# Optimization experiments

Hardware: AMD Instinct MI355X
Metric: run time of the kernel (lower is better)

## Reference

```python
import jax, jax.numpy as jnp
import numpy as np

B, H, W, C = 4, 64, 64, 256
D = C // 8  # out_channels // queries_ratio = 32


def setup_inputs() -> dict:
    key = jax.random.key(0)
    ks = jax.random.split(key, 8)
    s_in = 1.0 / np.sqrt(C)  # he_normal-ish scale for 1x1 convs
    s_d = 1.0 / np.sqrt(D)
    return {
        "x": jax.random.normal(ks[0], (B, H, W, C), dtype=jnp.float32),
        "Wk": jax.random.normal(ks[1], (C, D), dtype=jnp.float32) * s_in,
        "bk": jnp.zeros((D,), dtype=jnp.float32),
        "Wq": jax.random.normal(ks[2], (C, D), dtype=jnp.float32) * s_in,
        "bq": jnp.zeros((D,), dtype=jnp.float32),
        "Wv": jax.random.normal(ks[3], (C, D), dtype=jnp.float32) * s_in,
        "bv": jnp.zeros((D,), dtype=jnp.float32),
        "Wo": jax.random.normal(ks[4], (D, C), dtype=jnp.float32) * s_d,
        "bo": jnp.zeros((C,), dtype=jnp.float32),
        "gamma": jax.random.normal(ks[5], (1,), dtype=jnp.float32) * 0.1,
    }


def reference(x, Wk, bk, Wq, bq, Wv, bv, Wo, bo, gamma):
    b, h, w, c = x.shape
    n = h * w
    xf = x.reshape(b, n, c)  # flatten spatial -> [B, N, C]
    # 1x1 convs == per-position channel matmuls
    k = xf @ Wk + bk  # [B, N, D]
    q = xf @ Wq + bq  # [B, N, D]
    v = xf @ Wv + bv  # [B, N, D]
    energy = jnp.einsum('bnd,bmd->bnm', q, k)  # [B, N, N] (no scaling, as in source)
    attn = jax.nn.softmax(energy, axis=-1)
    feat = jnp.einsum('bnm,bmd->bnd', attn, v)  # [B, N, D]
    out = feat @ Wo + bo  # 1x1 output conv -> [B, N, C]
    out = gamma[0] * out + xf  # gamma scale + identity shortcut (C_in == C_out)
    return out.reshape(b, h, w, c)
```

## Files before the change

### kernel.cpp

```cpp
#include <hip/hip_runtime.h>
#include <hip/hip_bf16.h>
#include <hip/hip_fp16.h>


#define BB 4
#define NN 4096
#define CC 256
#define DD 32
#define LOG2E 1.44269504088896340736f
#define THR2 11.0f

typedef _Float16 half_t;
typedef _Float16 half2_t __attribute__((ext_vector_type(2)));
typedef _Float16 half4_t __attribute__((ext_vector_type(4)));
typedef _Float16 half8_t __attribute__((ext_vector_type(8)));
typedef float f32x4 __attribute__((ext_vector_type(4)));

#define MFMA_QK(a, b, c) __builtin_amdgcn_mfma_f32_16x16x32_f16(a, b, c, 0, 0, 0)
#define MFMA_PV(a, b, c) __builtin_amdgcn_mfma_f32_16x16x16f16(a, b, c, 0, 0, 0)

static __device__ inline float fexp2(float x) {
#if __has_builtin(__builtin_amdgcn_exp2f)
    return __builtin_amdgcn_exp2f(x);
#else
    return exp2f(x);
#endif
}

__global__ __launch_bounds__(256) void proj_kernel(
    const float* __restrict__ x,
    const float* __restrict__ Wk, const float* __restrict__ bk,
    const float* __restrict__ Wq, const float* __restrict__ bq,
    const float* __restrict__ Wv, const float* __restrict__ bv,
    half_t* __restrict__ k_ws, half_t* __restrict__ q_ws, half_t* __restrict__ vT2)
{
    __shared__ half_t xs16[32][264];
    __shared__ half_t Wt[96][264];

    const int t = threadIdx.x;
    const int row0 = blockIdx.x * 32;

    const float4* x4 = reinterpret_cast<const float4*>(x) + (size_t)row0 * 64;
    for (int idx = t; idx < 32 * 64; idx += 256) {
        int r = idx >> 6, c4 = idx & 63;
        float4 v = x4[r * 64 + c4];
        half4_t h;
        h[0] = (half_t)v.x; h[1] = (half_t)v.y; h[2] = (half_t)v.z; h[3] = (half_t)v.w;
        *reinterpret_cast<half4_t*>(&xs16[r][c4 * 4]) = h;
    }

    for (int idx = t; idx < 3072; idx += 256) {
        int cp = idx & 127;
        int rest = idx >> 7;
        int d4 = (rest & 7) * 4;
        int mat = rest >> 3;
        const float* Wm = (mat == 0) ? Wk : ((mat == 1) ? Wq : Wv);
        const float sc = (mat == 1) ? LOG2E : 1.0f;
        float4 w0 = *reinterpret_cast<const float4*>(Wm + (2 * cp) * DD + d4);
        float4 w1 = *reinterpret_cast<const float4*>(Wm + (2 * cp + 1) * DD + d4);
        int rbase = mat * 32 + d4;
        half2_t h;
        h[0] = (half_t)(w0.x * sc); h[1] = (half_t)(w1.x * sc);
        *reinterpret_cast<half2_t*>(&Wt[rbase + 0][2 * cp]) = h;
        h[0] = (half_t)(w0.y * sc); h[1] = (half_t)(w1.y * sc);
        *reinterpret_cast<half2_t*>(&Wt[rbase + 1][2 * cp]) = h;
        h[0] = (half_t)(w0.z * sc); h[1] = (half_t)(w1.z * sc);
        *reinterpret_cast<half2_t*>(&Wt[rbase + 2][2 * cp]) = h;
        h[0] = (half_t)(w0.w * sc); h[1] = (half_t)(w1.w * sc);
        *reinterpret_cast<half2_t*>(&Wt[rbase + 3][2 * cp]) = h;
    }
    __syncthreads();

    const int w = t >> 6, lane = t & 63;
    const int c = lane & 15, g = lane >> 4;
    const int rt = w >> 1;
    const int ct0 = (w & 1) * 3;

    f32x4 acc[3];
#pragma unroll
    for (int j = 0; j < 3; ++j) acc[j] = (f32x4){0.f, 0.f, 0.f, 0.f};

#pragma unroll
    for (int kk = 0; kk < 8; ++kk) {
        const int k0 = kk * 32 + g * 8;
        half8_t bfrag = *reinterpret_cast<const half8_t*>(&xs16[rt * 16 + c][k0]);
#pragma unroll
        for (int j = 0; j < 3; ++j) {
            half8_t afrag = *reinterpret_cast<const half8_t*>(&Wt[(ct0 + j) * 16 + c][k0]);
            acc[j] = MFMA_QK(afrag, bfrag, acc[j]);
        }
    }

    const int grow = row0 + rt * 16 + c;
#pragma unroll
    for (int j = 0; j < 3; ++j) {
        const int ct = ct0 + j;
        const int mat = ct >> 1;
        const float* bm = (mat == 0) ? bk : ((mat == 1) ? bq : bv);
        float4 bb = *reinterpret_cast<const float4*>(bm + (ct & 1) * 16 + g * 4);
        if (mat < 2) {
            const float bsc = (mat == 1) ? LOG2E : 1.0f;
            half_t* dst = (mat == 0) ? k_ws : q_ws;
            half4_t h;
            h[0] = (half_t)(acc[j][0] + bb.x * bsc);
            h[1] = (half_t)(acc[j][1] + bb.y * bsc);
            h[2] = (half_t)(acc[j][2] + bb.z * bsc);
            h[3] = (half_t)(acc[j][3] + bb.w * bsc);
            *reinterpret_cast<half4_t*>(dst + (size_t)grow * DD + (ct & 1) * 16 + g * 4) = h;
        } else {
            const size_t tbase = ((size_t)(row0 >> 4) + rt) * 512;
            const int d0 = (ct & 1) * 16 + g * 4;
            vT2[tbase + (size_t)(d0 + 0) * 16 + c] = (half_t)(acc[j][0] + bb.x);
            vT2[tbase + (size_t)(d0 + 1) * 16 + c] = (half_t)(acc[j][1] + bb.y);
            vT2[tbase + (size_t)(d0 + 2) * 16 + c] = (half_t)(acc[j][2] + bb.z);
            vT2[tbase + (size_t)(d0 + 3) * 16 + c] = (half_t)(acc[j][3] + bb.w);
        }
    }
}

__global__ __launch_bounds__(512) void attn_kernel(
    const half_t* __restrict__ k_ws, const half_t* __restrict__ q_ws,
    const half_t* __restrict__ vT2,
    const float* __restrict__ x, const float* __restrict__ Wo,
    const float* __restrict__ bo, const float* __restrict__ gamma,
    float* __restrict__ out)
{
    __shared__ float m_l[8][4][16];
    __shared__ float s_l[8][4][16];
    __shared__ float acc_l[8][64][4][8];
    __shared__ float feat_lds[64][32];

    const int tid = threadIdx.x;
    const int w = tid >> 6, lane = tid & 63;
    const int q = lane & 15, g = lane >> 4;
    const int b = blockIdx.x >> 6, qb = blockIdx.x & 63;
    const int q0 = qb * 64;

    half8_t qf[4];
#pragma unroll
    for (int t = 0; t < 4; ++t)
        qf[t] = *reinterpret_cast<const half8_t*>(
            q_ws + (size_t)(b * NN + q0 + t * 16 + q) * DD + g * 8);

    float m[4], ssum[4];
    f32x4 accd0[4], accd1[4];
#pragma unroll
    for (int t = 0; t < 4; ++t) {
        m[t] = -3.0e38f; ssum[t] = 0.f;
        accd0[t] = (f32x4){0.f, 0.f, 0.f, 0.f};
        accd1[t] = (f32x4){0.f, 0.f, 0.f, 0.f};
    }

    const half_t* kbase = k_ws + ((size_t)b * NN + q) * DD + g * 8;
    const half_t* vb = vT2 + (size_t)b * 256 * 512 + q * 16 + g * 4;

    const int ktbase = w * 32;

    half8_t kc0 = *reinterpret_cast<const half8_t*>(kbase + (size_t)(ktbase + 0) * 16 * DD);
    half8_t kc1 = *reinterpret_cast<const half8_t*>(kbase + (size_t)(ktbase + 1) * 16 * DD);
    half4_t va0 = *reinterpret_cast<const half4_t*>(vb + (size_t)(ktbase + 0) * 512);
    half4_t va1 = *reinterpret_cast<const half4_t*>(vb + (size_t)(ktbase + 0) * 512 + 256);
    half4_t vc0 = *reinterpret_cast<const half4_t*>(vb + (size_t)(ktbase + 1) * 512);
    half4_t vc1 = *reinterpret_cast<const half4_t*>(vb + (size_t)(ktbase + 1) * 512 + 256);

    for (int it = 0; it < 16; ++it) {
        const int kt = ktbase + it * 2;
        const int ktn = (it < 15) ? (kt + 2) : kt;

        half8_t kn0 = *reinterpret_cast<const half8_t*>(kbase + (size_t)(ktn + 0) * 16 * DD);
        half8_t kn1 = *reinterpret_cast<const half8_t*>(kbase + (size_t)(ktn + 1) * 16 * DD);
        half4_t wa0 = *reinterpret_cast<const half4_t*>(vb + (size_t)(ktn + 0) * 512);
        half4_t wa1 = *reinterpret_cast<const half4_t*>(vb + (size_t)(ktn + 0) * 512 + 256);
        half4_t wc0 = *reinterpret_cast<const half4_t*>(vb + (size_t)(ktn + 1) * 512);
        half4_t wc1 = *reinterpret_cast<const half4_t*>(vb + (size_t)(ktn + 1) * 512 + 256);

        f32x4 z = {0.f, 0.f, 0.f, 0.f};
        f32x4 s0[4], s1[4];
#pragma unroll
        for (int t = 0; t < 4; ++t) {
            s0[t] = MFMA_QK(kc0, qf[t], z);
            s1[t] = MFMA_QK(kc1, qf[t], z);
        }

        float tmax[4];
        bool need = false;
#pragma unroll
        for (int t = 0; t < 4; ++t) {
            float t0 = fmaxf(fmaxf(s0[t][0], s0[t][1]), fmaxf(s0[t][2], s0[t][3]));
            float t1 = fmaxf(fmaxf(s1[t][0], s1[t][1]), fmaxf(s1[t][2], s1[t][3]));
            tmax[t] = fmaxf(t0, t1);
            need = need || (tmax[t] > m[t] + THR2);
        }

        if (__any(need)) {
#pragma unroll
            for (int t = 0; t < 4; ++t) {
                float rmax = tmax[t];
                rmax = fmaxf(rmax, __shfl_xor(rmax, 16));
                rmax = fmaxf(rmax, __shfl_xor(rmax, 32));
                float mn = fmaxf(m[t], rmax);
                float sc = fexp2(m[t] - mn);
                ssum[t] *= sc;
                accd0[t] *= sc;
                accd1[t] *= sc;
                m[t] = mn;
            }
        }

#pragma unroll
        for (int t = 0; t < 4; ++t) {
            float p00 = fexp2(s0[t][0] - m[t]), p01 = fexp2(s0[t][1] - m[t]);
            float p02 = fexp2(s0[t][2] - m[t]), p03 = fexp2(s0[t][3] - m[t]);
            float p10 = fexp2(s1[t][0] - m[t]), p11 = fexp2(s1[t][1] - m[t]);
            float p12 = fexp2(s1[t][2] - m[t]), p13 = fexp2(s1[t][3] - m[t]);
            ssum[t] += ((p00 + p01) + (p02 + p03)) + ((p10 + p11) + (p12 + p13));

            half4_t pf0, pf1;
            pf0[0] = (half_t)p00; pf0[1] = (half_t)p01; pf0[2] = (half_t)p02; pf0[3] = (half_t)p03;
            pf1[0] = (half_t)p10; pf1[1] = (half_t)p11; pf1[2] = (half_t)p12; pf1[3] = (half_t)p13;

            accd0[t] = MFMA_PV(va0, pf0, accd0[t]);
            accd1[t] = MFMA_PV(va1, pf0, accd1[t]);
            accd0[t] = MFMA_PV(vc0, pf1, accd0[t]);
            accd1[t] = MFMA_PV(vc1, pf1, accd1[t]);
        }

        kc0 = kn0; kc1 = kn1;
        va0 = wa0; va1 = wa1; vc0 = wc0; vc1 = wc1;
    }

#pragma unroll
    for (int t = 0; t < 4; ++t) {
        ssum[t] += __shfl_xor(ssum[t], 16);
        ssum[t] += __shfl_xor(ssum[t], 32);
    }

    if (lane < 16) {
#pragma unroll
        for (int t = 0; t < 4; ++t) { m_l[w][t][lane] = m[t]; s_l[w][t][lane] = ssum[t]; }
    }
#pragma unroll
    for (int t = 0; t < 4; ++t)
#pragma unroll
        for (int i = 0; i < 4; ++i) {
            acc_l[w][lane][t][i] = accd0[t][i];
            acc_l[w][lane][t][4 + i] = accd1[t][i];
        }
    __syncthreads();

    if (w < 4) {
        const int t = w;
        float M = m_l[0][t][q];
#pragma unroll
        for (int ww = 1; ww < 8; ++ww) M = fmaxf(M, m_l[ww][t][q]);
        float SS = 0.f;
        float f[8] = {0.f, 0.f, 0.f, 0.f, 0.f, 0.f, 0.f, 0.f};
#pragma unroll
        for (int ww = 0; ww < 8; ++ww) {
            float sc = fexp2(m_l[ww][t][q] - M);
            SS += s_l[ww][t][q] * sc;
#pragma unroll
            for (int i = 0; i < 8; ++i) f[i] += acc_l[ww][lane][t][i] * sc;
        }
        float inv = 1.0f / SS;
#pragma unroll
        for (int i = 0; i < 4; ++i) {
            feat_lds[t * 16 + q][g * 4 + i] = f[i] * inv;
            feat_lds[t * 16 + q][16 + g * 4 + i] = f[4 + i] * inv;
        }
    }
    __syncthreads();

    const int c = tid & 255, rh = tid >> 8;
    float wv[32];
#pragma unroll
    for (int d = 0; d < DD; ++d) wv[d] = Wo[d * CC + c];
    const float gam = gamma[0];
    const float bias = bo[c];

#pragma unroll
    for (int chunk = 0; chunk < 4; ++chunk) {
        const int r0 = rh * 32 + chunk * 8;
        float oacc[8] = {0.f, 0.f, 0.f, 0.f, 0.f, 0.f, 0.f, 0.f};
#pragma unroll
        for (int d = 0; d < DD; ++d) {
            float wvd = wv[d];
#pragma unroll
            for (int r = 0; r < 8; ++r) oacc[r] += feat_lds[r0 + r][d] * wvd;
        }
        const size_t base = ((size_t)b * NN + (size_t)q0 + r0) * CC + c;
        const float* xr = x + base;
        float* outr = out + base;
#pragma unroll
        for (int r = 0; r < 8; ++r)
            outr[(size_t)r * CC] = gam * (oacc[r] + bias) + xr[(size_t)r * CC];
    }
}

extern "C" void kernel_launch(void* const* d_in, const int* in_sizes, int n_in,
                              void* d_out, int out_size, void* d_ws, size_t ws_size,
                              hipStream_t stream) {
    const float* x  = (const float*)d_in[0];
    const float* Wk = (const float*)d_in[1];
    const float* bk = (const float*)d_in[2];
    const float* Wq = (const float*)d_in[3];
    const float* bq = (const float*)d_in[4];
    const float* Wv = (const float*)d_in[5];
    const float* bv = (const float*)d_in[6];
    const float* Wo = (const float*)d_in[7];
    const float* bo = (const float*)d_in[8];
    const float* gamma = (const float*)d_in[9];
    float* out = (float*)d_out;

    half_t* k_ws  = (half_t*)d_ws;
    half_t* q_ws  = k_ws + (size_t)BB * NN * DD;
    half_t* vT2   = q_ws + (size_t)BB * NN * DD;

    proj_kernel<<<512, 256, 0, stream>>>(x, Wk, bk, Wq, bq, Wv, bv, k_ws, q_ws, vT2);
    attn_kernel<<<256, 512, 0, stream>>>(k_ws, q_ws, vT2, x, Wo, bo, gamma, out);
}
```

Before: 46.50 us.

## Use MFMA for output projection and double proj kernel rows per block

The attention epilogue now stages Wo transposed in fp16 in shared memory and computes the output 1x1 conv with 16x16x32 MFMA instructions instead of scalar FMAs. It also writes float4-vectorized output. The per-wave accumulator buffer is padded to reduce LDS bank conflicts. The projection kernel handles 64 rows per block with 512 threads, which halves the number of times the weights are staged. The costs are fp16 rounding of feat and Wo, extra LDS use, and the hidden proj compute loop must match the new thread count.

After: 40.38 us. 1.15x faster.

```diff
diff --git a/kernel.cpp b/kernel.cpp
--- a/kernel.cpp
+++ b/kernel.cpp
@@ -27,21 +27,21 @@
 #endif
 }
 
-__global__ __launch_bounds__(256) void proj_kernel(
+__global__ __launch_bounds__(512) void proj_kernel(
     const float* __restrict__ x,
     const float* __restrict__ Wk, const float* __restrict__ bk,
     const float* __restrict__ Wq, const float* __restrict__ bq,
     const float* __restrict__ Wv, const float* __restrict__ bv,
     half_t* __restrict__ k_ws, half_t* __restrict__ q_ws, half_t* __restrict__ vT2)
 {
-    __shared__ half_t xs16[32][264];
+    __shared__ half_t xs16[64][264];
     __shared__ half_t Wt[96][264];
 
     const int t = threadIdx.x;
-    const int row0 = blockIdx.x * 32;
+    const int row0 = blockIdx.x * 64;
 
     const float4* x4 = reinterpret_cast<const float4*>(x) + (size_t)row0 * 64;
-    for (int idx = t; idx < 32 * 64; idx += 256) {
+    for (int idx = t; idx < 64 * 64; idx += 512) {
         int r = idx >> 6, c4 = idx & 63;
         float4 v = x4[r * 64 + c4];
         half4_t h;
@@ -49,7 +49,7 @@
         *reinterpret_cast<half4_t*>(&xs16[r][c4 * 4]) = h;
     }
 
-    for (int idx = t; idx < 3072; idx += 256) {
+    for (int idx = t; idx < 3072; idx += 512) {
         int cp = idx & 127;
         int rest = idx >> 7;
         int d4 = (rest & 7) * 4;
@@ -125,16 +125,24 @@
     const float* __restrict__ bo, const float* __restrict__ gamma,
     float* __restrict__ out)
 {
+    __shared__ float acc_l[8][64][33];
     __shared__ float m_l[8][4][16];
     __shared__ float s_l[8][4][16];
-    __shared__ float acc_l[8][64][4][8];
-    __shared__ float feat_lds[64][32];
+    __shared__ half_t feat_h[64 * 40];
+    __shared__ half_t woT[256 * 40];
 
     const int tid = threadIdx.x;
     const int w = tid >> 6, lane = tid & 63;
     const int q = lane & 15, g = lane >> 4;
     const int b = blockIdx.x >> 6, qb = blockIdx.x & 63;
     const int q0 = qb * 64;
+
+#pragma unroll
+    for (int it = 0; it < 16; ++it) {
+        int idx = tid + it * 512;
+        int c = idx & 255, d = idx >> 8;
+        woT[c * 40 + d] = (half_t)Wo[d * CC + c];
+    }
 
     half8_t qf[4];
 #pragma unroll
@@ -243,8 +251,8 @@
     for (int t = 0; t < 4; ++t)
 #pragma unroll
         for (int i = 0; i < 4; ++i) {
-            acc_l[w][lane][t][i] = accd0[t][i];
-            acc_l[w][lane][t][4 + i] = accd1[t][i];
+            acc_l[w][lane][t * 8 + i] = accd0[t][i];
+            acc_l[w][lane][t * 8 + 4 + i] = accd1[t][i];
         }
     __syncthreads();
 
@@ -260,40 +268,37 @@
             float sc = fexp2(m_l[ww][t][q] - M);
             SS += s_l[ww][t][q] * sc;
 #pragma unroll
-            for (int i = 0; i < 8; ++i) f[i] += acc_l[ww][lane][t][i] * sc;
+            for (int i = 0; i < 8; ++i) f[i] += acc_l[ww][lane][t * 8 + i] * sc;
         }
         float inv = 1.0f / SS;
-#pragma unroll
-        for (int i = 0; i < 4; ++i) {
-            feat_lds[t * 16 + q][g * 4 + i] = f[i] * inv;
-            feat_lds[t * 16 + q][16 + g * 4 + i] = f[4 + i] * inv;
-        }
+        half4_t h0, h1;
+#pragma unroll
+        for (int i = 0; i < 4; ++i) { h0[i] = (half_t)(f[i] * inv); h1[i] = (half_t)(f[4 + i] * inv); }
+        *reinterpret_cast<half4_t*>(&feat_h[(t * 16 + q) * 40 + g * 4]) = h0;
+        *reinterpret_cast<half4_t*>(&feat_h[(t * 16 + q) * 40 + 16 + g * 4]) = h1;
     }
     __syncthreads();
 
-    const int c = tid & 255, rh = tid >> 8;
-    float wv[32];
-#pragma unroll
-    for (int d = 0; d < DD; ++d) wv[d] = Wo[d * CC + c];
     const float gam = gamma[0];
-    const float bias = bo[c];
-
-#pragma unroll
-    for (int chunk = 0; chunk < 4; ++chunk) {
-        const int r0 = rh * 32 + chunk * 8;
-        float oacc[8] = {0.f, 0.f, 0.f, 0.f, 0.f, 0.f, 0.f, 0.f};
-#pragma unroll
-        for (int d = 0; d < DD; ++d) {
-            float wvd = wv[d];
-#pragma unroll
-            for (int r = 0; r < 8; ++r) oacc[r] += feat_lds[r0 + r][d] * wvd;
-        }
-        const size_t base = ((size_t)b * NN + (size_t)q0 + r0) * CC + c;
-        const float* xr = x + base;
-        float* outr = out + base;
-#pragma unroll
-        for (int r = 0; r < 8; ++r)
-            outr[(size_t)r * CC] = gam * (oacc[r] + bias) + xr[(size_t)r * CC];
+#pragma unroll
+    for (int j = 0; j < 2; ++j) {
+        const int ct = w * 2 + j;
+        half8_t kfe = *reinterpret_cast<const half8_t*>(&woT[(ct * 16 + q) * 40 + g * 8]);
+        float4 bb4 = *reinterpret_cast<const float4*>(bo + ct * 16 + g * 4);
+#pragma unroll
+        for (int rt = 0; rt < 4; ++rt) {
+            half8_t qfe = *reinterpret_cast<const half8_t*>(&feat_h[(rt * 16 + q) * 40 + g * 8]);
+            f32x4 z = {0.f, 0.f, 0.f, 0.f};
+            f32x4 o = MFMA_QK(kfe, qfe, z);
+            const size_t base = ((size_t)b * NN + q0 + rt * 16 + q) * CC + ct * 16 + g * 4;
+            float4 xv = *reinterpret_cast<const float4*>(x + base);
+            float4 ov;
+            ov.x = gam * (o[0] + bb4.x) + xv.x;
+            ov.y = gam * (o[1] + bb4.y) + xv.y;
+            ov.z = gam * (o[2] + bb4.z) + xv.z;
+            ov.w = gam * (o[3] + bb4.w) + xv.w;
+            *reinterpret_cast<float4*>(out + base) = ov;
+        }
     }
 }
 
@@ -316,6 +321,6 @@
     half_t* q_ws  = k_ws + (size_t)BB * NN * DD;
     half_t* vT2   = q_ws + (size_t)BB * NN * DD;
 
-    proj_kernel<<<512, 256, 0, stream>>>(x, Wk, bk, Wq, bq, Wv, bv, k_ws, q_ws, vT2);
+    proj_kernel<<<256, 512, 0, stream>>>(x, Wk, bk, Wq, bq, Wv, bv, k_ws, q_ws, vT2);
     attn_kernel<<<256, 512, 0, stream>>>(k_ws, q_ws, vT2, x, Wo, bo, gamma, out);
 }
```
